# Performance work log

Measured on AMD Instinct MI355X. Metric: run time of the kernel, lower is better.

The kernel has to match this reference:

```python
import jax, jax.numpy as jnp
import numpy as np

NEG_SLOPE = 0.2  # PyG GATConv default leaky_relu slope

def gat_conv(x, src, dst, W, att_src, att_dst, bias, concat):
    # x: [N, F_in]; W: [F_in, H*D]; att_*: [H, D]; edges src->dst
    N = x.shape[0]
    H, D = att_src.shape
    h = (x @ W).reshape(N, H, D)                      # [N, H, D]
    a_src = (h * att_src[None]).sum(-1)               # [N, H]
    a_dst = (h * att_dst[None]).sum(-1)               # [N, H]
    e = jax.nn.leaky_relu(a_src[src] + a_dst[dst], NEG_SLOPE)  # [E, H]
    # segment softmax over incoming edges of each destination node
    emax = jax.ops.segment_max(e, dst, num_segments=N)          # [N, H]
    emax = jnp.where(jnp.isfinite(emax), emax, 0.0)
    ex = jnp.exp(e - emax[dst])                                  # [E, H]
    denom = jax.ops.segment_sum(ex, dst, num_segments=N)        # [N, H]
    alpha = ex / (denom[dst] + 1e-16)                            # [E, H]
    msg = h[src] * alpha[:, :, None]                             # [E, H, D]
    out = jax.ops.segment_sum(msg, dst, num_segments=N)          # [N, H, D]
    out = out.reshape(N, H * D) if concat else out.mean(axis=1)
    return out + bias

def setup_inputs() -> dict:
    key = jax.random.key(0)
    ks = jax.random.split(key, 10)
    N, F_in, E, H, D, C = 100000, 128, 3200000, 8, 8, 7
    x = jax.random.normal(ks[0], (N, F_in), jnp.float32)
    edge_index = jax.random.randint(ks[1], (2, E), 0, N, jnp.int64)
    W1 = jax.random.normal(ks[2], (F_in, H * D), jnp.float32) / np.sqrt(F_in)
    att_src1 = jax.random.normal(ks[3], (H, D), jnp.float32) / np.sqrt(D)
    att_dst1 = jax.random.normal(ks[4], (H, D), jnp.float32) / np.sqrt(D)
    b1 = jax.random.normal(ks[5], (H * D,), jnp.float32) * 0.01
    W2 = jax.random.normal(ks[6], (H * D, C), jnp.float32) / np.sqrt(H * D)
    att_src2 = jax.random.normal(ks[7], (1, C), jnp.float32) / np.sqrt(C)
    att_dst2 = jax.random.normal(ks[8], (1, C), jnp.float32) / np.sqrt(C)
    b2 = jax.random.normal(ks[9], (C,), jnp.float32) * 0.01
    return {"x": x, "edge_index": edge_index, "W1": W1, "att_src1": att_src1,
            "att_dst1": att_dst1, "b1": b1, "W2": W2, "att_src2": att_src2,
            "att_dst2": att_dst2, "b2": b2}

def reference(x, edge_index, W1, att_src1, att_dst1, b1, W2, att_src2, att_dst2, b2):
    N = x.shape[0]
    # PyG GATConv add_self_loops=True
    loop = jnp.arange(N, dtype=edge_index.dtype)
    src = jnp.concatenate([edge_index[0], loop])
    dst = jnp.concatenate([edge_index[1], loop])
    # eval mode: dropouts are no-ops
    h = gat_conv(x, src, dst, W1, att_src1, att_dst1, b1, concat=True)
    emb = h
    h = jax.nn.elu(h)
    logits = gat_conv(h, src, dst, W2, att_src2, att_dst2, b2, concat=False)
    return emb, jax.nn.log_softmax(logits, axis=1)
```

## Files before the change

kernel.cpp:

```cpp
#include <hip/hip_runtime.h>
#include <hip/hip_bf16.h>
#include <math.h>

#define F_IN 128
#define HD   64
#define NH   8
#define DH   8
#define NC   7

__device__ __forceinline__ float lrelu(float e) { return fmaxf(e, 0.2f * e); }
__device__ __forceinline__ ushort f2bf(float f) {
    unsigned u = __float_as_uint(f);
    unsigned rounded = u + 0x7FFF + ((u >> 16) & 1);
    return (ushort)(rounded >> 16);
}

__global__ __launch_bounds__(256) void k_gemm1h(
    const float* __restrict__ x, const float* __restrict__ W1,
    const float* __restrict__ att_src, const float* __restrict__ att_dst,
    ushort* __restrict__ h1b, float* __restrict__ a_src, float* __restrict__ a_dst,
    int N, int GB,
    const int* __restrict__ dstArr, int* __restrict__ deg, int* __restrict__ rank,
    long E)
{
    __shared__ float sX[64 * F_IN];
    int t = threadIdx.x;
    int bid = blockIdx.x;

    if (bid % 3 != 0) {
        long hb = (long)(bid / 3) * 2 + (bid % 3) - 1;
        long stride = (long)(2 * GB) * 256;
        for (long i = hb * 256 + t; i < E; i += stride)
            rank[i] = atomicAdd(&deg[dstArr[i]], 1);
        return;
    }

    int gb = bid / 3;
    int lane = t & 63;
    int wave = t >> 6;

    {
        float4 xv[8];
        int r0b = gb * 64;
        #pragma unroll
        for (int i = 0; i < 8; ++i) {
            int ch = i * 256 + t;
            int rr = r0b + (ch >> 5);
            if (rr >= N) rr = N - 1;
            xv[i] = *(const float4*)(x + (size_t)rr * F_IN + ((ch & 31) << 2));
        }
        #pragma unroll
        for (int i = 0; i < 8; ++i) {
            int ch = i * 256 + t;
            *(float4*)(sX + ch * 4) = xv[i];
        }
    }
    float asv = att_src[lane];
    float adv = att_dst[lane];
    __syncthreads();

    int base = gb * 64 + wave * 16;

    #pragma unroll 1
    for (int it = 0; it < 2; ++it) {
        int r0 = base + it * 8;
        if (r0 >= N) break;
        int nr = N - r0; if (nr > 8) nr = 8;
        int lr = wave * 16 + it * 8;

        float acc[8];
        #pragma unroll
        for (int r = 0; r < 8; ++r) acc[r] = 0.f;

        #pragma unroll 1
        for (int kh = 0; kh < 2; ++kh) {
            float wreg[64];
            #pragma unroll
            for (int k = 0; k < 64; ++k)
                wreg[k] = W1[(kh * 64 + k) * HD + lane];

            const float* xb = sX + lr * F_IN + kh * 64;
            #pragma unroll
            for (int k4 = 0; k4 < 16; ++k4) {
                float4 xv[8];
                #pragma unroll
                for (int r = 0; r < 8; ++r)
                    xv[r] = *(const float4*)(xb + r * F_IN + k4 * 4);
                #pragma unroll
                for (int kk = 0; kk < 4; ++kk) {
                    float w = wreg[k4 * 4 + kk];
                    acc[0] += ((const float*)&xv[0])[kk] * w;
                    acc[1] += ((const float*)&xv[1])[kk] * w;
                    acc[2] += ((const float*)&xv[2])[kk] * w;
                    acc[3] += ((const float*)&xv[3])[kk] * w;
                    acc[4] += ((const float*)&xv[4])[kk] * w;
                    acc[5] += ((const float*)&xv[5])[kk] * w;
                    acc[6] += ((const float*)&xv[6])[kk] * w;
                    acc[7] += ((const float*)&xv[7])[kk] * w;
                }
            }
        }

        #pragma unroll
        for (int r = 0; r < 8; ++r) {
            if (r < nr) {
                int row = r0 + r;
                float a = acc[r];
                h1b[(size_t)row * HD + lane] = f2bf(a);
                float vs = a * asv;
                float vd = a * adv;
                #pragma unroll
                for (int o = 4; o > 0; o >>= 1) {
                    vs += __shfl_down(vs, o, 8);
                    vd += __shfl_down(vd, o, 8);
                }
                if ((lane & 7) == 0) {
                    int h = lane >> 3;
                    a_src[row * NH + h] = vs;
                    a_dst[row * NH + h] = vd;
                }
            }
        }
    }
}

__global__ __launch_bounds__(256) void k_bsum(
    const int* __restrict__ deg, int* __restrict__ bsum, int N)
{
    __shared__ int s[256];
    int t = threadIdx.x;
    int i = blockIdx.x * 256 + t;
    s[t] = (i < N) ? deg[i] : 0;
    __syncthreads();
    #pragma unroll
    for (int o = 128; o > 0; o >>= 1) {
        if (t < o) s[t] += s[t + o];
        __syncthreads();
    }
    if (t == 0) bsum[blockIdx.x] = s[0];
}

__global__ __launch_bounds__(512) void k_scan_bsum(
    const int* __restrict__ bsum, int* __restrict__ bexc, int NB)
{
    __shared__ int s[512];
    int t = threadIdx.x;
    s[t] = (t < NB) ? bsum[t] : 0;
    __syncthreads();
    for (int o = 1; o < 512; o <<= 1) {
        int v = (t >= o) ? s[t - o] : 0;
        __syncthreads();
        s[t] += v;
        __syncthreads();
    }
    if (t < NB) bexc[t] = (t == 0) ? 0 : s[t - 1];
}

__global__ __launch_bounds__(256) void k_rowptr(
    const int* __restrict__ deg, const int* __restrict__ bexc,
    int* __restrict__ rowptr, int N, int Etot)
{
    __shared__ int s[256];
    int t = threadIdx.x;
    int i = blockIdx.x * 256 + t;
    int v = (i < N) ? deg[i] : 0;
    s[t] = v;
    __syncthreads();
    for (int o = 1; o < 256; o <<= 1) {
        int u = (t >= o) ? s[t - o] : 0;
        __syncthreads();
        s[t] += u;
        __syncthreads();
    }
    if (i < N) rowptr[i] = bexc[blockIdx.x] + s[t] - v;
    if (i == 0) rowptr[N] = Etot;
}

__global__ __launch_bounds__(256) void k_fill(
    const int* __restrict__ src, const int* __restrict__ dst,
    const int* __restrict__ rank, const int* __restrict__ rowptr,
    int* __restrict__ csr, long E)
{
    long i4 = ((long)blockIdx.x * 256 + threadIdx.x) * 4;
    if (i4 >= E) return;
    if (i4 + 3 < E) {
        int4 d4 = *(const int4*)(dst + i4);
        int4 r4 = *(const int4*)(rank + i4);
        int4 s4 = *(const int4*)(src + i4);
        int p0 = rowptr[d4.x], p1 = rowptr[d4.y];
        int p2 = rowptr[d4.z], p3 = rowptr[d4.w];
        csr[p0 + r4.x] = s4.x;
        csr[p1 + r4.y] = s4.y;
        csr[p2 + r4.z] = s4.z;
        csr[p3 + r4.w] = s4.w;
    } else {
        for (long i = i4; i < E; ++i)
            csr[rowptr[dst[i]] + rank[i]] = src[i];
    }
}

__global__ __launch_bounds__(256) void k_gather1(
    const int* __restrict__ rowptr, const int* __restrict__ csr,
    const ushort* __restrict__ h1b, const float* __restrict__ a_src,
    const float* __restrict__ a_dst, float* __restrict__ agg, int N)
{
    const uint* __restrict__ h1u = (const uint*)h1b;
    int wave = threadIdx.x >> 6, lane = threadIdx.x & 63;
    int d = blockIdx.x * 4 + wave;
    if (d >= N) return;
    int e = lane >> 3;
    int h = lane & 7;

    float adst = a_dst[d * NH + h];
    float ws = __expf(lrelu(a_src[d * NH + h] + adst));
    float wsum = (e == 0) ? ws : 0.f;

    float ax0 = 0.f, ay0 = 0.f, ax1 = 0.f, ay1 = 0.f;
    float ax2 = 0.f, ay2 = 0.f, ax3 = 0.f, ay3 = 0.f;
    if (e == 0) {
        size_t b = (size_t)d * 32 + h * 4;
        uint u0 = h1u[b], u1 = h1u[b + 1], u2 = h1u[b + 2], u3 = h1u[b + 3];
        ax0 = ws * __uint_as_float(u0 << 16); ay0 = ws * __uint_as_float(u0 & 0xFFFF0000u);
        ax1 = ws * __uint_as_float(u1 << 16); ay1 = ws * __uint_as_float(u1 & 0xFFFF0000u);
        ax2 = ws * __uint_as_float(u2 << 16); ay2 = ws * __uint_as_float(u2 & 0xFFFF0000u);
        ax3 = ws * __uint_as_float(u3 << 16); ay3 = ws * __uint_as_float(u3 & 0xFFFF0000u);
    }

    int jb = rowptr[d], je = rowptr[d + 1];

    int  idx0 = jb + e;
    bool v0   = idx0 < je;
    int  sl0  = v0 ? csr[idx0] : d;
    float as0 = a_src[sl0 * NH + h];
    size_t b0 = (size_t)sl0 * 32 + h * 4;
    uint u0 = h1u[b0], u1 = h1u[b0 + 1], u2 = h1u[b0 + 2], u3 = h1u[b0 + 3];

    int  idx1 = jb + 8 + e;
    bool v1   = idx1 < je;
    int  sl1  = v1 ? csr[idx1] : d;
    float as1 = a_src[sl1 * NH + h];

    int  idx2 = jb + 16 + e;
    bool v2   = idx2 < je;
    int  sl2  = v2 ? csr[idx2] : d;

    for (int j0 = jb; j0 < je; j0 += 8) {
        int  idx3 = j0 + 24 + e;
        bool v3   = idx3 < je;
        int  sl3  = v3 ? csr[idx3] : d;
        float as2 = a_src[sl2 * NH + h];
        size_t b1 = (size_t)sl1 * 32 + h * 4;
        uint n0 = h1u[b1], n1 = h1u[b1 + 1], n2 = h1u[b1 + 2], n3 = h1u[b1 + 3];

        float w = v0 ? __expf(lrelu(as0 + adst)) : 0.f;
        wsum += w;
        ax0 += w * __uint_as_float(u0 << 16); ay0 += w * __uint_as_float(u0 & 0xFFFF0000u);
        ax1 += w * __uint_as_float(u1 << 16); ay1 += w * __uint_as_float(u1 & 0xFFFF0000u);
        ax2 += w * __uint_as_float(u2 << 16); ay2 += w * __uint_as_float(u2 & 0xFFFF0000u);
        ax3 += w * __uint_as_float(u3 << 16); ay3 += w * __uint_as_float(u3 & 0xFFFF0000u);

        v0 = v1; as0 = as1; u0 = n0; u1 = n1; u2 = n2; u3 = n3;
        v1 = v2; sl1 = sl2; as1 = as2;
        v2 = v3; sl2 = sl3;
    }

    #pragma unroll
    for (int o = 8; o <= 32; o <<= 1) {
        wsum += __shfl_xor(wsum, o, 64);
        ax0 += __shfl_xor(ax0, o, 64); ay0 += __shfl_xor(ay0, o, 64);
        ax1 += __shfl_xor(ax1, o, 64); ay1 += __shfl_xor(ay1, o, 64);
        ax2 += __shfl_xor(ax2, o, 64); ay2 += __shfl_xor(ay2, o, 64);
        ax3 += __shfl_xor(ax3, o, 64); ay3 += __shfl_xor(ay3, o, 64);
    }
    if (e == 0) {
        float winv = 1.f / (wsum + 1e-16f);
        float* op = agg + (size_t)d * HD + h * 8;
        *(float4*)(op)     = make_float4(ax0 * winv, ay0 * winv, ax1 * winv, ay1 * winv);
        *(float4*)(op + 4) = make_float4(ax2 * winv, ay2 * winv, ax3 * winv, ay3 * winv);
    }
}

__global__ __launch_bounds__(256) void k_node2(
    const float* __restrict__ agg1, const float* __restrict__ b1,
    const float* __restrict__ W2, const float* __restrict__ att_s2,
    const float* __restrict__ att_d2, float* __restrict__ emb_out,
    float* __restrict__ h2p, float* __restrict__ a_src2, float* __restrict__ a_dst2,
    int N)
{
    __shared__ float sW[HD * NC];
    __shared__ float sb[HD];
    __shared__ float sas[NC], sad[NC];
    int t = threadIdx.x;
    for (int i = t; i < HD * NC; i += 256) sW[i] = W2[i];
    if (t < HD) sb[t] = b1[t];
    if (t < NC) { sas[t] = att_s2[t]; sad[t] = att_d2[t]; }
    __syncthreads();
    int n = blockIdx.x * 256 + t;
    if (n >= N) return;
    const float* ag = agg1 + (size_t)n * HD;
    float* eo = emb_out + (size_t)n * HD;
    float acc[NC];
    #pragma unroll
    for (int c = 0; c < NC; ++c) acc[c] = 0.f;
    #pragma unroll 8
    for (int k = 0; k < HD; ++k) {
        float v = ag[k] + sb[k];
        eo[k] = v;
        float xv = v > 0.f ? v : expm1f(v);
        #pragma unroll
        for (int c = 0; c < NC; ++c) acc[c] += xv * sW[k * NC + c];
    }
    float as = 0.f, ad = 0.f;
    float* hp = h2p + (size_t)n * 8;
    #pragma unroll
    for (int c = 0; c < NC; ++c) {
        hp[c] = acc[c];
        as += acc[c] * sas[c];
        ad += acc[c] * sad[c];
    }
    hp[7] = 0.f;
    a_src2[n] = as;
    a_dst2[n] = ad;
}

__global__ __launch_bounds__(256) void k_gather2(
    const int* __restrict__ rowptr, const int* __restrict__ csr,
    const float* __restrict__ h2p, const float* __restrict__ a_src2,
    const float* __restrict__ a_dst2, const float* __restrict__ b2,
    float* __restrict__ out, int N)
{
    int t = threadIdx.x;
    int wave = t >> 6, lane = t & 63;
    int g = lane >> 3;
    int c = lane & 7;
    int n = blockIdx.x * 4 + wave;
    if (n >= N) return;
    float ad = a_dst2[n];
    float w = __expf(lrelu(a_src2[n] + ad));
    float acc  = (g == 0) ? w * h2p[(size_t)n * 8 + c] : 0.f;
    float wsum = (g == 0) ? w : 0.f;
    int jb = rowptr[n], je = rowptr[n + 1];

    int  idx0 = jb + g;
    bool v0   = idx0 < je;
    int  s0   = v0 ? csr[idx0] : n;
    float as0 = a_src2[s0];
    float hv0 = h2p[(size_t)s0 * 8 + c];

    int  idx1 = jb + 8 + g;
    bool v1   = idx1 < je;
    int  s1   = v1 ? csr[idx1] : n;

    for (int j = jb; j < je; j += 8) {
        int  idx2 = j + 16 + g;
        bool v2   = idx2 < je;
        int  s2   = v2 ? csr[idx2] : n;
        float as1 = a_src2[s1];
        float hv1 = h2p[(size_t)s1 * 8 + c];
        float ww = v0 ? __expf(lrelu(as0 + ad)) : 0.f;
        acc += ww * hv0;
        wsum += ww;
        v0 = v1; as0 = as1; hv0 = hv1;
        v1 = v2; s1 = s2;
    }
    #pragma unroll
    for (int o = 32; o >= 8; o >>= 1) {
        acc  += __shfl_xor(acc, o, 64);
        wsum += __shfl_xor(wsum, o, 64);
    }
    float l = (c < NC) ? (acc / (wsum + 1e-16f) + b2[c]) : -1e30f;
    float m = l;
    #pragma unroll
    for (int o = 4; o > 0; o >>= 1) m = fmaxf(m, __shfl_xor(m, o, 8));
    float ex = (c < NC) ? __expf(l - m) : 0.f;
    float s8 = ex;
    #pragma unroll
    for (int o = 4; o > 0; o >>= 1) s8 += __shfl_xor(s8, o, 8);
    if (g == 0 && c < NC) out[(size_t)n * NC + c] = l - m - logf(s8);
}

extern "C" void kernel_launch(void* const* d_in, const int* in_sizes, int n_in,
                              void* d_out, int out_size, void* d_ws, size_t ws_size,
                              hipStream_t stream)
{
    const float* x       = (const float*)d_in[0];
    const int*   ei      = (const int*)d_in[1];
    const float* W1      = (const float*)d_in[2];
    const float* att_s1  = (const float*)d_in[3];
    const float* att_d1  = (const float*)d_in[4];
    const float* b1      = (const float*)d_in[5];
    const float* W2      = (const float*)d_in[6];
    const float* att_s2  = (const float*)d_in[7];
    const float* att_d2  = (const float*)d_in[8];
    const float* b2      = (const float*)d_in[9];

    const int  N = in_sizes[0] / F_IN;
    const long E = (long)in_sizes[1] / 2;
    const int* src = ei;
    const int* dst = ei + E;

    const int Npad  = (N + 3) & ~3;
    const int Np1p  = (N + 4) & ~3;
    const long Epad = (E + 3) & ~3;

    int* deg    = (int*)d_ws;
    int* rowptr = deg + Npad;
    int* bexc   = rowptr + Np1p;
    int* bsum   = bexc + 512;
    int* csr    = bsum + 512;
    ushort* h1b   = (ushort*)(csr + Epad);
    float* a_src1 = (float*)(h1b + (size_t)Npad * HD);
    float* a_dst1 = a_src1 + (size_t)N * NH;
    float* agg1   = a_dst1 + (size_t)N * NH;
    float* h2p    = agg1 + (size_t)N * HD;
    float* a_src2 = h2p + (size_t)N * 8;
    float* a_dst2 = a_src2 + Npad;
    float* wsend  = a_dst2 + Npad;
    int* rank = (E <= (long)N * HD) ? (int*)agg1 : (int*)wsend;

    hipMemsetAsync(deg, 0, (size_t)Npad * sizeof(int), stream);

    const int NB = (N + 255) / 256;
    const int GB = (N + 63) / 64;
    dim3 b256(256);

    k_gemm1h<<<dim3(3 * GB), b256, 0, stream>>>(
        x, W1, att_s1, att_d1, h1b, a_src1, a_dst1, N, GB,
        dst, deg, rank, E);
    k_bsum<<<dim3(NB), b256, 0, stream>>>(deg, bsum, N);
    k_scan_bsum<<<dim3(1), dim3(512), 0, stream>>>(bsum, bexc, NB);
    k_rowptr<<<dim3(NB), b256, 0, stream>>>(deg, bexc, rowptr, N, (int)E);
    k_fill<<<dim3((unsigned)((E + 1023) / 1024)), b256, 0, stream>>>(
        src, dst, rank, rowptr, csr, E);

    k_gather1<<<dim3((N + 3) / 4), b256, 0, stream>>>(
        rowptr, csr, h1b, a_src1, a_dst1, agg1, N);

    float* emb = (float*)d_out;
    float* lsm = emb + (size_t)N * HD;
    k_node2<<<dim3(NB), b256, 0, stream>>>(
        agg1, b1, W2, att_s2, att_d2, emb, h2p, a_src2, a_dst2, N);

    k_gather2<<<dim3((N + 3) / 4), b256, 0, stream>>>(
        rowptr, csr, h2p, a_src2, a_dst2, b2, lsm, N);
}
```

Before: 633.5 us.

## Replicate degree counters to spread atomic contention in CSR build

The degree-counting atomics now go to one of eight replicated degree arrays, chosen by edge group, and each thread loads four destinations with a vectorized int4 load. A per-replica exclusive prefix is computed in k_bsum and added in k_fill to place each edge in its CSR slot. The goal is to cut atomic contention on shared counters and raise memory-level parallelism. In exchange it adds a larger memset, eight times the degree reads and writes, an extra lookup per edge in the fill step, and reuses workspace buffers (h2p, agg1) as scratch.

```diff
diff --git a/kernel.cpp b/kernel.cpp
--- a/kernel.cpp
+++ b/kernel.cpp
@@ -7,6 +7,7 @@
 #define NH   8
 #define DH   8
 #define NC   7
+#define NREP 8
 
 __device__ __forceinline__ float lrelu(float e) { return fmaxf(e, 0.2f * e); }
 __device__ __forceinline__ ushort f2bf(float f) {
@@ -19,8 +20,8 @@
     const float* __restrict__ x, const float* __restrict__ W1,
     const float* __restrict__ att_src, const float* __restrict__ att_dst,
     ushort* __restrict__ h1b, float* __restrict__ a_src, float* __restrict__ a_dst,
-    int N, int GB,
-    const int* __restrict__ dstArr, int* __restrict__ deg, int* __restrict__ rank,
+    int N, int Npad, int GB,
+    const int* __restrict__ dstArr, int* __restrict__ deg_r, int* __restrict__ rank,
     long E)
 {
     __shared__ float sX[64 * F_IN];
@@ -29,9 +30,24 @@
 
     if (bid % 3 != 0) {
         long hb = (long)(bid / 3) * 2 + (bid % 3) - 1;
-        long stride = (long)(2 * GB) * 256;
-        for (long i = hb * 256 + t; i < E; i += stride)
-            rank[i] = atomicAdd(&deg[dstArr[i]], 1);
+        long gstride = (long)(2 * GB) * 1024;
+        for (long base0 = hb * 1024; base0 < E; base0 += gstride) {
+            long base = base0 + (long)t * 4;
+            if (base >= E) continue;
+            int r = (int)((base >> 2) & (NREP - 1));
+            int* dg = deg_r + (size_t)r * Npad;
+            if (base + 3 < E) {
+                int4 d4 = *(const int4*)(dstArr + base);
+                int r0_ = atomicAdd(&dg[d4.x], 1);
+                int r1_ = atomicAdd(&dg[d4.y], 1);
+                int r2_ = atomicAdd(&dg[d4.z], 1);
+                int r3_ = atomicAdd(&dg[d4.w], 1);
+                *(int4*)(rank + base) = make_int4(r0_, r1_, r2_, r3_);
+            } else {
+                for (long i = base; i < E; ++i)
+                    rank[i] = atomicAdd(&dg[dstArr[i]], 1);
+            }
+        }
         return;
     }
 
@@ -125,12 +141,23 @@
 }
 
 __global__ __launch_bounds__(256) void k_bsum(
-    const int* __restrict__ deg, int* __restrict__ bsum, int N)
+    const int* __restrict__ deg_r, int* __restrict__ pre,
+    int* __restrict__ deg_total, int* __restrict__ bsum, int N, int Npad)
 {
     __shared__ int s[256];
     int t = threadIdx.x;
     int i = blockIdx.x * 256 + t;
-    s[t] = (i < N) ? deg[i] : 0;
+    int tot = 0;
+    if (i < N) {
+        #pragma unroll
+        for (int r = 0; r < NREP; ++r) {
+            int v = deg_r[(size_t)r * Npad + i];
+            pre[(size_t)r * Npad + i] = tot;
+            tot += v;
+        }
+        deg_total[i] = tot;
+    }
+    s[t] = tot;
     __syncthreads();
     #pragma unroll
     for (int o = 128; o > 0; o >>= 1) {
@@ -179,23 +206,28 @@
 __global__ __launch_bounds__(256) void k_fill(
     const int* __restrict__ src, const int* __restrict__ dst,
     const int* __restrict__ rank, const int* __restrict__ rowptr,
-    int* __restrict__ csr, long E)
+    const int* __restrict__ pre, int* __restrict__ csr, int Npad, long E)
 {
     long i4 = ((long)blockIdx.x * 256 + threadIdx.x) * 4;
     if (i4 >= E) return;
+    const int* pr = pre + (size_t)((i4 >> 2) & (NREP - 1)) * Npad;
     if (i4 + 3 < E) {
         int4 d4 = *(const int4*)(dst + i4);
         int4 r4 = *(const int4*)(rank + i4);
         int4 s4 = *(const int4*)(src + i4);
-        int p0 = rowptr[d4.x], p1 = rowptr[d4.y];
-        int p2 = rowptr[d4.z], p3 = rowptr[d4.w];
+        int p0 = rowptr[d4.x] + pr[d4.x];
+        int p1 = rowptr[d4.y] + pr[d4.y];
+        int p2 = rowptr[d4.z] + pr[d4.z];
+        int p3 = rowptr[d4.w] + pr[d4.w];
         csr[p0 + r4.x] = s4.x;
         csr[p1 + r4.y] = s4.y;
         csr[p2 + r4.z] = s4.z;
         csr[p3 + r4.w] = s4.w;
     } else {
-        for (long i = i4; i < E; ++i)
-            csr[rowptr[dst[i]] + rank[i]] = src[i];
+        for (long i = i4; i < E; ++i) {
+            int d = dst[i];
+            csr[rowptr[d] + pr[d] + rank[i]] = src[i];
+        }
     }
 }
 
@@ -403,8 +435,8 @@
     const int Np1p  = (N + 4) & ~3;
     const long Epad = (E + 3) & ~3;
 
-    int* deg    = (int*)d_ws;
-    int* rowptr = deg + Npad;
+    int* deg_total = (int*)d_ws;
+    int* rowptr = deg_total + Npad;
     int* bexc   = rowptr + Np1p;
     int* bsum   = bexc + 512;
     int* csr    = bsum + 512;
@@ -416,22 +448,24 @@
     float* a_src2 = h2p + (size_t)N * 8;
     float* a_dst2 = a_src2 + Npad;
     float* wsend  = a_dst2 + Npad;
-    int* rank = (E <= (long)N * HD) ? (int*)agg1 : (int*)wsend;
-
-    hipMemsetAsync(deg, 0, (size_t)Npad * sizeof(int), stream);
+    int* deg_r = (int*)h2p;
+    int* rank  = (int*)agg1;
+    int* pre   = (int*)agg1 + Epad;
+
+    hipMemsetAsync(deg_r, 0, (size_t)NREP * Npad * sizeof(int), stream);
 
     const int NB = (N + 255) / 256;
     const int GB = (N + 63) / 64;
     dim3 b256(256);
 
     k_gemm1h<<<dim3(3 * GB), b256, 0, stream>>>(
-        x, W1, att_s1, att_d1, h1b, a_src1, a_dst1, N, GB,
-        dst, deg, rank, E);
-    k_bsum<<<dim3(NB), b256, 0, stream>>>(deg, bsum, N);
+        x, W1, att_s1, att_d1, h1b, a_src1, a_dst1, N, Npad, GB,
+        dst, deg_r, rank, E);
+    k_bsum<<<dim3(NB), b256, 0, stream>>>(deg_r, pre, deg_total, bsum, N, Npad);
     k_scan_bsum<<<dim3(1), dim3(512), 0, stream>>>(bsum, bexc, NB);
-    k_rowptr<<<dim3(NB), b256, 0, stream>>>(deg, bexc, rowptr, N, (int)E);
+    k_rowptr<<<dim3(NB), b256, 0, stream>>>(deg_total, bexc, rowptr, N, (int)E);
     k_fill<<<dim3((unsigned)((E + 1023) / 1024)), b256, 0, stream>>>(
-        src, dst, rank, rowptr, csr, E);
+        src, dst, rank, rowptr, pre, csr, Npad, E);
 
     k_gather1<<<dim3((N + 3) / 4), b256, 0, stream>>>(
         rowptr, csr, h1b, a_src1, a_dst1, agg1, N);
```

Result: slower. 647.1 us (+2.2%).

## Compute first-layer GEMM with split-bf16 MFMA instead of scalar FP32 FMAs

Applied to the files above, without the earlier changes.

Replaces the shared-memory FP32 scalar GEMM for x@W1 with MFMA 16x16x32 bf16 instructions. It uses a three-term hi/lo bf16 split to keep near-FP32 accuracy. A new single-block kernel pre-splits W1 into hi/lo bf16 fragments in the MFMA operand layout, stored in scratch space reused from a_src2. This removes the LDS staging and the per-lane FP32 FMA loop, at the cost of an extra launch and three MFMAs per tile.

```diff
diff --git a/kernel.cpp b/kernel.cpp
--- a/kernel.cpp
+++ b/kernel.cpp
@@ -8,6 +8,9 @@
 #define DH   8
 #define NC   7
 
+typedef __attribute__((ext_vector_type(8))) short short8v;
+typedef __attribute__((ext_vector_type(4))) float f32x4;
+
 __device__ __forceinline__ float lrelu(float e) { return fmaxf(e, 0.2f * e); }
 __device__ __forceinline__ ushort f2bf(float f) {
     unsigned u = __float_as_uint(f);
@@ -15,15 +18,32 @@
     return (ushort)(rounded >> 16);
 }
 
+__global__ __launch_bounds__(256) void k_wcvt(
+    const float* __restrict__ W1, ushort* __restrict__ Wh, ushort* __restrict__ Wl)
+{
+    int t = threadIdx.x;
+    for (int g = t; g < 8192; g += 256) {
+        int i = g & 7, lane = (g >> 3) & 63, fs = g >> 9;
+        int ct = fs >> 2, ks = fs & 3;
+        int k = (ks << 5) + ((lane >> 4) << 3) + i;
+        int c = (ct << 4) + (lane & 15);
+        float w = W1[k * HD + c];
+        ushort wh = f2bf(w);
+        float whf = __uint_as_float((uint)wh << 16);
+        Wh[g] = wh;
+        Wl[g] = f2bf(w - whf);
+    }
+}
+
 __global__ __launch_bounds__(256) void k_gemm1h(
-    const float* __restrict__ x, const float* __restrict__ W1,
+    const float* __restrict__ x,
+    const ushort* __restrict__ Wh, const ushort* __restrict__ Wl,
     const float* __restrict__ att_src, const float* __restrict__ att_dst,
     ushort* __restrict__ h1b, float* __restrict__ a_src, float* __restrict__ a_dst,
     int N, int GB,
     const int* __restrict__ dstArr, int* __restrict__ deg, int* __restrict__ rank,
     long E)
 {
-    __shared__ float sX[64 * F_IN];
     int t = threadIdx.x;
     int bid = blockIdx.x;
 
@@ -38,87 +58,63 @@
     int gb = bid / 3;
     int lane = t & 63;
     int wave = t >> 6;
-
-    {
-        float4 xv[8];
-        int r0b = gb * 64;
+    int base = gb * 64 + wave * 16;
+    if (base >= N) return;
+
+    int arow = base + (lane & 15);
+    if (arow >= N) arow = N - 1;
+    int kg = lane >> 4;
+
+    f32x4 acc[4];
+    #pragma unroll
+    for (int ct = 0; ct < 4; ++ct) acc[ct] = (f32x4){0.f, 0.f, 0.f, 0.f};
+
+    #pragma unroll
+    for (int ks = 0; ks < 4; ++ks) {
+        const float* xp = x + (size_t)arow * F_IN + ks * 32 + kg * 8;
+        float4 xa = *(const float4*)xp;
+        float4 xb = *(const float4*)(xp + 4);
+        float xs[8] = {xa.x, xa.y, xa.z, xa.w, xb.x, xb.y, xb.z, xb.w};
+        short8v ah, al;
         #pragma unroll
         for (int i = 0; i < 8; ++i) {
-            int ch = i * 256 + t;
-            int rr = r0b + (ch >> 5);
-            if (rr >= N) rr = N - 1;
-            xv[i] = *(const float4*)(x + (size_t)rr * F_IN + ((ch & 31) << 2));
+            ushort hh = f2bf(xs[i]);
+            ah[i] = (short)hh;
+            float hf = __uint_as_float((uint)hh << 16);
+            al[i] = (short)f2bf(xs[i] - hf);
         }
         #pragma unroll
-        for (int i = 0; i < 8; ++i) {
-            int ch = i * 256 + t;
-            *(float4*)(sX + ch * 4) = xv[i];
+        for (int ct = 0; ct < 4; ++ct) {
+            size_t fo = (size_t)((ct * 4 + ks) * 64 + lane) * 8;
+            short8v bh = *(const short8v*)(Wh + fo);
+            short8v bl = *(const short8v*)(Wl + fo);
+            acc[ct] = __builtin_amdgcn_mfma_f32_16x16x32_bf16(ah, bh, acc[ct], 0, 0, 0);
+            acc[ct] = __builtin_amdgcn_mfma_f32_16x16x32_bf16(al, bh, acc[ct], 0, 0, 0);
+            acc[ct] = __builtin_amdgcn_mfma_f32_16x16x32_bf16(ah, bl, acc[ct], 0, 0, 0);
         }
     }
-    float asv = att_src[lane];
-    float adv = att_dst[lane];
-    __syncthreads();
-
-    int base = gb * 64 + wave * 16;
-
-    #pragma unroll 1
-    for (int it = 0; it < 2; ++it) {
-        int r0 = base + it * 8;
-        if (r0 >= N) break;
-        int nr = N - r0; if (nr > 8) nr = 8;
-        int lr = wave * 16 + it * 8;
-
-        float acc[8];
+
+    int rg = lane >> 4;
+    int cl = lane & 15;
+    #pragma unroll
+    for (int ct = 0; ct < 4; ++ct) {
+        int c = ct * 16 + cl;
+        float asv = att_src[c];
+        float adv = att_dst[c];
         #pragma unroll
-        for (int r = 0; r < 8; ++r) acc[r] = 0.f;
-
-        #pragma unroll 1
-        for (int kh = 0; kh < 2; ++kh) {
-            float wreg[64];
-            #pragma unroll
-            for (int k = 0; k < 64; ++k)
-                wreg[k] = W1[(kh * 64 + k) * HD + lane];
-
-            const float* xb = sX + lr * F_IN + kh * 64;
-            #pragma unroll
-            for (int k4 = 0; k4 < 16; ++k4) {
-                float4 xv[8];
-                #pragma unroll
-                for (int r = 0; r < 8; ++r)
-                    xv[r] = *(const float4*)(xb + r * F_IN + k4 * 4);
-                #pragma unroll
-                for (int kk = 0; kk < 4; ++kk) {
-                    float w = wreg[k4 * 4 + kk];
-                    acc[0] += ((const float*)&xv[0])[kk] * w;
-                    acc[1] += ((const float*)&xv[1])[kk] * w;
-                    acc[2] += ((const float*)&xv[2])[kk] * w;
-                    acc[3] += ((const float*)&xv[3])[kk] * w;
-                    acc[4] += ((const float*)&xv[4])[kk] * w;
-                    acc[5] += ((const float*)&xv[5])[kk] * w;
-                    acc[6] += ((const float*)&xv[6])[kk] * w;
-                    acc[7] += ((const float*)&xv[7])[kk] * w;
-                }
-            }
-        }
-
-        #pragma unroll
-        for (int r = 0; r < 8; ++r) {
-            if (r < nr) {
-                int row = r0 + r;
-                float a = acc[r];
-                h1b[(size_t)row * HD + lane] = f2bf(a);
-                float vs = a * asv;
-                float vd = a * adv;
-                #pragma unroll
-                for (int o = 4; o > 0; o >>= 1) {
-                    vs += __shfl_down(vs, o, 8);
-                    vd += __shfl_down(vd, o, 8);
-                }
-                if ((lane & 7) == 0) {
-                    int h = lane >> 3;
-                    a_src[row * NH + h] = vs;
-                    a_dst[row * NH + h] = vd;
-                }
+        for (int r = 0; r < 4; ++r) {
+            int row = base + rg * 4 + r;
+            float v = acc[ct][r];
+            if (row < N) h1b[(size_t)row * HD + c] = f2bf(v);
+            float vs = v * asv;
+            float vd = v * adv;
+            vs += __shfl_xor(vs, 1, 64); vd += __shfl_xor(vd, 1, 64);
+            vs += __shfl_xor(vs, 2, 64); vd += __shfl_xor(vd, 2, 64);
+            vs += __shfl_xor(vs, 4, 64); vd += __shfl_xor(vd, 4, 64);
+            if ((lane & 7) == 0 && row < N) {
+                int head = 2 * ct + ((lane >> 3) & 1);
+                a_src[row * NH + head] = vs;
+                a_dst[row * NH + head] = vd;
             }
         }
     }
@@ -417,6 +413,8 @@
     float* a_dst2 = a_src2 + Npad;
     float* wsend  = a_dst2 + Npad;
     int* rank = (E <= (long)N * HD) ? (int*)agg1 : (int*)wsend;
+    ushort* Wh = (ushort*)a_src2;
+    ushort* Wl = Wh + 8192;
 
     hipMemsetAsync(deg, 0, (size_t)Npad * sizeof(int), stream);
 
@@ -424,8 +422,10 @@
     const int GB = (N + 63) / 64;
     dim3 b256(256);
 
+    k_wcvt<<<dim3(1), b256, 0, stream>>>(W1, Wh, Wl);
+
     k_gemm1h<<<dim3(3 * GB), b256, 0, stream>>>(
-        x, W1, att_s1, att_d1, h1b, a_src1, a_dst1, N, GB,
+        x, Wh, Wl, att_s1, att_d1, h1b, a_src1, a_dst1, N, GB,
         dst, deg, rank, E);
     k_bsum<<<dim3(NB), b256, 0, stream>>>(deg, bsum, N);
     k_scan_bsum<<<dim3(1), dim3(512), 0, stream>>>(bsum, bexc, NB);
```

After: 626.2 us. Within noise of the previous version (-1.1%).
